# Kernel optimization log

Measured on AMD Instinct MI355X. Metric: run time of the kernel, lower is better.

Reference implementation:

```python
import jax, jax.numpy as jnp
import numpy as np

KH, KW = 15, 15
H, W = 4096, 4096


def setup_inputs() -> dict:
    key = jax.random.key(0)
    kx, kw = jax.random.split(key)
    x = jax.random.normal(kx, (H, W), dtype=jnp.float32)
    weight = jax.random.uniform(kw, (KH, KW), dtype=jnp.float32)
    bias = jnp.zeros((1,), dtype=jnp.float32)
    return {"x": x, "weight": weight, "bias": bias}


def reference(x, weight, bias):
    # corr2d: valid 2D cross-correlation of [H,W] input with [kh,kw] kernel,
    # output [H-kh+1, W-kw+1], plus scalar bias.
    lhs = x[None, None, :, :]            # [1,1,H,W]
    rhs = weight[None, None, :, :]       # [1,1,kh,kw]
    out = jax.lax.conv_general_dilated(
        lhs, rhs,
        window_strides=(1, 1),
        padding="VALID",
        dimension_numbers=("NCHW", "OIHW", "NCHW"),
    )[0, 0]                              # [H-kh+1, W-kw+1]
    return out + bias[0]
```

## Files before the change

### kernel.cpp

```cpp
#include <hip/hip_runtime.h>

typedef short bf16x8 __attribute__((ext_vector_type(8)));
typedef float f32x4  __attribute__((ext_vector_type(4)));

static constexpr int KH = 15, KW = 15;
static constexpr int HI = 4096, WI = 4096;
static constexpr int HO = HI - KH + 1, WO = WI - KW + 1;
static constexpr int TM = 64, TN = 128;
static constexpr int NT = 2;
static constexpr int LR   = TM + KH - 1;
static constexpr int LC   = 144;
static constexpr int LSTR = 152;
static constexpr int IPR   = LC / 4;
static constexpr int ITEMS = LR * IPR;
static constexpr int SITER = (ITEMS + 511) / 512;
static constexpr int NSLOT = 23;
static constexpr int BKH   = NSLOT * 8;

__device__ __forceinline__ unsigned int f2bf(float f) {
  unsigned int u = __builtin_bit_cast(unsigned int, f);
  return (u + 0x7FFFu + ((u >> 16) & 1u)) >> 16;
}

__device__ __forceinline__ unsigned int cvt_pk_bf16(float lo, float hi) {
  unsigned int r;
  asm("v_cvt_pk_bf16_f32 %0, %1, %2" : "=v"(r) : "v"(lo), "v"(hi));
  return r;
}

__device__ __forceinline__ float4 load_item(const float* __restrict__ x,
                                            int row0, int col0, int it) {
  float4 v = make_float4(0.f, 0.f, 0.f, 0.f);
  if (it < ITEMS) {
    const int r  = it / IPR;
    const int c4 = (it - r * IPR) * 4;
    const int gr = row0 + r;
    const int gc = col0 + c4;
    if (gr < HI) {
      const float* p = &x[(long)gr * WI + gc];
      if (gc + 3 < WI) {
        v = *(const float4*)p;
      } else {
        if (gc + 0 < WI) v.x = p[0];
        if (gc + 1 < WI) v.y = p[1];
        if (gc + 2 < WI) v.z = p[2];
        if (gc + 3 < WI) v.w = p[3];
      }
    }
  }
  return v;
}

__device__ __forceinline__ void write_item(unsigned short* sx, int it, float4 v) {
  if (it < ITEMS) {
    const int r  = it / IPR;
    const int c4 = (it - r * IPR) * 4;
    *(uint2*)&sx[r * LSTR + c4] = make_uint2(cvt_pk_bf16(v.x, v.y), cvt_pk_bf16(v.z, v.w));
  }
}

#define MFMA16(a, b, c) __builtin_amdgcn_mfma_f32_16x16x32_bf16((a), (b), (c), 0, 0, 0)

__global__ __launch_bounds__(512, 4)
void conv2d_m2(const float* __restrict__ x, const float* __restrict__ w,
               const float* __restrict__ bias, float* __restrict__ out) {
  __shared__ unsigned short sx[LR * LSTR];
  __shared__ unsigned short btab[KH * BKH];

  const int tid = threadIdx.x;

  const int bid0  = blockIdx.y * gridDim.x + blockIdx.x;
  const int bid   = (bid0 & 7) * 128 + (bid0 >> 3);
  const int col0  = (bid & 31) * TN;
  const int rbase = (bid >> 5) * (NT * TM);

  for (int i = tid; i < KH * NSLOT; i += 512) {
    const int kh = i / NSLOT;
    const int s  = i - kh * NSLOT;
    const int e0 = s - 7;
    unsigned int dw[4];
    #pragma unroll
    for (int t2 = 0; t2 < 4; ++t2) {
      const int c0 = e0 + 2 * t2;
      const int c1 = c0 + 1;
      const unsigned int b0 = (c0 >= 0 && c0 < KW) ? f2bf(w[kh * KW + c0]) : 0u;
      const unsigned int b1 = (c1 >= 0 && c1 < KW) ? f2bf(w[kh * KW + c1]) : 0u;
      dw[t2] = b0 | (b1 << 16);
    }
    *(uint4*)&btab[i * 8] = make_uint4(dw[0], dw[1], dw[2], dw[3]);
  }

  {
    float4 v0_[SITER];
    #pragma unroll
    for (int k = 0; k < SITER; ++k) v0_[k] = load_item(x, rbase, col0, tid + 512 * k);
    #pragma unroll
    for (int k = 0; k < SITER; ++k) write_item(sx, tid + 512 * k, v0_[k]);
  }
  const float bs = bias[0];
  __syncthreads();

  const int lane = tid & 63;
  const int wv   = tid >> 6;
  const int q    = lane & 15;
  const int kg4  = lane >> 4;
  const unsigned short* abase = &sx[q * LSTR + wv * 16 + kg4 * 8];
  const int e    = 8 * kg4 - q;
  const int s    = (e >= -7 && e <= 14) ? e + 7 : 22;
  const unsigned short* bbase = &btab[s * 8];
  const int ocol = col0 + wv * 16 + q;

  #pragma unroll
  for (int t = 0; t < NT; ++t) {
    const int row0 = rbase + t * TM;

    float4 nv[SITER];
    if (t + 1 < NT) {
      #pragma unroll
      for (int k = 0; k < SITER; ++k)
        nv[k] = load_item(x, row0 + TM, col0, tid + 512 * k);
    }

    f32x4 acc0 = {bs,bs,bs,bs}, acc1 = {bs,bs,bs,bs};
    f32x4 acc2 = {bs,bs,bs,bs}, acc3 = {bs,bs,bs,bs};
    __builtin_amdgcn_s_setprio(1);
    #pragma unroll
    for (int kh = 0; kh < 15; ++kh) {
      const bf16x8 b = *(const bf16x8*)(bbase + kh * BKH);
      const unsigned short* ar = abase + kh * LSTR;
      acc0 = MFMA16(*(const bf16x8*)(ar + 0  * LSTR), b, acc0);
      acc1 = MFMA16(*(const bf16x8*)(ar + 16 * LSTR), b, acc1);
      acc2 = MFMA16(*(const bf16x8*)(ar + 32 * LSTR), b, acc2);
      acc3 = MFMA16(*(const bf16x8*)(ar + 48 * LSTR), b, acc3);
    }
    __builtin_amdgcn_s_setprio(0);

    if (ocol < WO) {
      const int orb = row0 + kg4 * 4;
      const f32x4 av[4] = {acc0, acc1, acc2, acc3};
      #pragma unroll
      for (int m = 0; m < 4; ++m) {
        #pragma unroll
        for (int r = 0; r < 4; ++r) {
          const int orow = orb + 16 * m + r;
          if (orow < HO) out[(long)orow * WO + ocol] = av[m][r];
        }
      }
    }

    if (t + 1 < NT) {
      __syncthreads();
      #pragma unroll
      for (int k = 0; k < SITER; ++k) write_item(sx, tid + 512 * k, nv[k]);
      __syncthreads();
    }
  }
}

extern "C" void kernel_launch(void* const* d_in, const int* in_sizes, int n_in,
                              void* d_out, int out_size, void* d_ws, size_t ws_size,
                              hipStream_t stream) {
  const float* x    = (const float*)d_in[0];
  const float* w    = (const float*)d_in[1];
  const float* bias = (const float*)d_in[2];
  float* out        = (float*)d_out;

  dim3 grid(32, 32);
  conv2d_m2<<<grid, dim3(512, 1, 1), 0, stream>>>(x, w, bias, out);
}
```

Before: 34.94 us.

## Swap MFMA operands so output is row-major per lane, hoist weights to registers

Swaps the MFMA A/B operands so that the weight fragment becomes A and the input tile becomes B. Each lane then holds four consecutive output columns of one row and can store them as two float2 writes instead of scattered scalar stores. The 15 weight fragments are preloaded into registers once. The shared tile gets an 8-element skew every 16 rows to avoid LDS bank conflicts with the new access pattern. The prefetch of the next tile's global loads is moved after compute, which removes the load/compute overlap and reduces register pressure.

```diff
diff --git a/kernel.cpp b/kernel.cpp
--- a/kernel.cpp
+++ b/kernel.cpp
@@ -16,6 +16,8 @@
 static constexpr int SITER = (ITEMS + 511) / 512;
 static constexpr int NSLOT = 23;
 static constexpr int BKH   = NSLOT * 8;
+
+__device__ __forceinline__ int rowbase(int r) { return r * LSTR + ((r >> 4) << 3); }
 
 __device__ __forceinline__ unsigned int f2bf(float f) {
   unsigned int u = __builtin_bit_cast(unsigned int, f);
@@ -55,16 +57,16 @@
   if (it < ITEMS) {
     const int r  = it / IPR;
     const int c4 = (it - r * IPR) * 4;
-    *(uint2*)&sx[r * LSTR + c4] = make_uint2(cvt_pk_bf16(v.x, v.y), cvt_pk_bf16(v.z, v.w));
+    *(uint2*)&sx[rowbase(r) + c4] = make_uint2(cvt_pk_bf16(v.x, v.y), cvt_pk_bf16(v.z, v.w));
   }
 }
 
 #define MFMA16(a, b, c) __builtin_amdgcn_mfma_f32_16x16x32_bf16((a), (b), (c), 0, 0, 0)
 
 __global__ __launch_bounds__(512, 4)
-void conv2d_m2(const float* __restrict__ x, const float* __restrict__ w,
+void conv2d_tr(const float* __restrict__ x, const float* __restrict__ w,
                const float* __restrict__ bias, float* __restrict__ out) {
-  __shared__ unsigned short sx[LR * LSTR];
+  __shared__ unsigned short sx[LR * LSTR + 64];
   __shared__ unsigned short btab[KH * BKH];
 
   const int tid = threadIdx.x;
@@ -102,53 +104,61 @@
 
   const int lane = tid & 63;
   const int wv   = tid >> 6;
-  const int q    = lane & 15;
+  const int l15  = lane & 15;
   const int kg4  = lane >> 4;
-  const unsigned short* abase = &sx[q * LSTR + wv * 16 + kg4 * 8];
-  const int e    = 8 * kg4 - q;
-  const int s    = (e >= -7 && e <= 14) ? e + 7 : 22;
-  const unsigned short* bbase = &btab[s * 8];
-  const int ocol = col0 + wv * 16 + q;
+
+  const int e = 8 * kg4 - l15;
+  const int s = (e >= -7 && e <= 14) ? e + 7 : 22;
+  bf16x8 wf[KH];
+  #pragma unroll
+  for (int kh = 0; kh < KH; ++kh)
+    wf[kh] = *(const bf16x8*)&btab[s * 8 + kh * BKH];
+
+  const int colsh = wv * 16 + kg4 * 8;
+  const int ocb   = col0 + wv * 16 + kg4 * 4;
 
   #pragma unroll
   for (int t = 0; t < NT; ++t) {
-    const int row0 = rbase + t * TM;
-
-    float4 nv[SITER];
-    if (t + 1 < NT) {
-      #pragma unroll
-      for (int k = 0; k < SITER; ++k)
-        nv[k] = load_item(x, row0 + TM, col0, tid + 512 * k);
-    }
+    const int trow0 = rbase + t * TM;
 
     f32x4 acc0 = {bs,bs,bs,bs}, acc1 = {bs,bs,bs,bs};
     f32x4 acc2 = {bs,bs,bs,bs}, acc3 = {bs,bs,bs,bs};
+
     __builtin_amdgcn_s_setprio(1);
     #pragma unroll
     for (int kh = 0; kh < 15; ++kh) {
-      const bf16x8 b = *(const bf16x8*)(bbase + kh * BKH);
-      const unsigned short* ar = abase + kh * LSTR;
-      acc0 = MFMA16(*(const bf16x8*)(ar + 0  * LSTR), b, acc0);
-      acc1 = MFMA16(*(const bf16x8*)(ar + 16 * LSTR), b, acc1);
-      acc2 = MFMA16(*(const bf16x8*)(ar + 32 * LSTR), b, acc2);
-      acc3 = MFMA16(*(const bf16x8*)(ar + 48 * LSTR), b, acc3);
+      const unsigned short* ar = &sx[rowbase(l15 + kh) + colsh];
+      acc0 = MFMA16(wf[kh], *(const bf16x8*)(ar + 0 * (16 * LSTR + 8)), acc0);
+      acc1 = MFMA16(wf[kh], *(const bf16x8*)(ar + 1 * (16 * LSTR + 8)), acc1);
+      acc2 = MFMA16(wf[kh], *(const bf16x8*)(ar + 2 * (16 * LSTR + 8)), acc2);
+      acc3 = MFMA16(wf[kh], *(const bf16x8*)(ar + 3 * (16 * LSTR + 8)), acc3);
     }
     __builtin_amdgcn_s_setprio(0);
 
-    if (ocol < WO) {
-      const int orb = row0 + kg4 * 4;
+    {
       const f32x4 av[4] = {acc0, acc1, acc2, acc3};
       #pragma unroll
       for (int m = 0; m < 4; ++m) {
-        #pragma unroll
-        for (int r = 0; r < 4; ++r) {
-          const int orow = orb + 16 * m + r;
-          if (orow < HO) out[(long)orow * WO + ocol] = av[m][r];
+        const int orow = trow0 + 16 * m + l15;
+        if (orow < HO) {
+          float* po = &out[(long)orow * WO + ocb];
+          if (ocb + 3 < WO) {
+            *(float2*)(po + 0) = make_float2(av[m][0], av[m][1]);
+            *(float2*)(po + 2) = make_float2(av[m][2], av[m][3]);
+          } else {
+            #pragma unroll
+            for (int r = 0; r < 4; ++r)
+              if (ocb + r < WO) po[r] = av[m][r];
+          }
         }
       }
     }
 
     if (t + 1 < NT) {
+      float4 nv[SITER];
+      #pragma unroll
+      for (int k = 0; k < SITER; ++k)
+        nv[k] = load_item(x, trow0 + TM, col0, tid + 512 * k);
       __syncthreads();
       #pragma unroll
       for (int k = 0; k < SITER; ++k) write_item(sx, tid + 512 * k, nv[k]);
@@ -166,5 +176,5 @@
   float* out        = (float*)d_out;
 
   dim3 grid(32, 32);
-  conv2d_m2<<<grid, dim3(512, 1, 1), 0, stream>>>(x, w, bias, out);
+  conv2d_tr<<<grid, dim3(512, 1, 1), 0, stream>>>(x, w, bias, out);
 }
```

Result: slower. 38.95 us (+11.5%).
